# Optimization experiments

Hardware: AMD Instinct MI355X
Metric: run time of the kernel (lower is better)

## Reference

```python
import jax, jax.numpy as jnp
import numpy as np

B, C, H, W = 16, 256, 64, 64
C8, C2 = C // 8, C // 2


def conv1x1(x, w, b):
    # x: [B,Cin,H,W], w: [Cout,Cin], b: [Cout]
    return jnp.einsum('oc,bchw->bohw', w, x) + b[None, :, None, None]


def maxpool2(x):
    # 2x2 max pool, stride 2. x: [B,C,H,W] -> [B,C,H//2,W//2]
    b, c, h, w = x.shape
    return x.reshape(b, c, h // 2, 2, w // 2, 2).max(axis=(3, 5))


def setup_inputs() -> dict:
    key = jax.random.key(0)
    ks = jax.random.split(key, 9)
    s = lambda fan_in: 1.0 / np.sqrt(fan_in)
    return {
        'x': jax.random.normal(ks[0], (B, C, H, W), jnp.float32),
        'w_theta': jax.random.normal(ks[1], (C8, C), jnp.float32) * s(C),
        'b_theta': jax.random.normal(ks[2], (C8,), jnp.float32) * 0.01,
        'w_phi': jax.random.normal(ks[3], (C8, C), jnp.float32) * s(C),
        'b_phi': jax.random.normal(ks[4], (C8,), jnp.float32) * 0.01,
        'w_g': jax.random.normal(ks[5], (C2, C), jnp.float32) * s(C),
        'b_g': jax.random.normal(ks[6], (C2,), jnp.float32) * 0.01,
        'w_o': jax.random.normal(ks[7], (C, C2), jnp.float32) * s(C2),
        'b_o': jax.random.normal(ks[8], (C,), jnp.float32) * 0.01,
        'gamma': jnp.full((1,), 0.5, jnp.float32),
    }


def reference(x, w_theta, b_theta, w_phi, b_phi, w_g, b_g, w_o, b_o, gamma):
    b, c, h, w = x.shape
    n, m = h * w, (h * w) // 4
    theta = conv1x1(x, w_theta, b_theta).reshape(b, C8, n)        # [B,C/8,N]
    phi = maxpool2(conv1x1(x, w_phi, b_phi)).reshape(b, C8, m)    # [B,C/8,M]
    g = maxpool2(conv1x1(x, w_g, b_g)).reshape(b, C2, m)          # [B,C/2,M]
    # beta = softmax(theta^T phi) over keys M
    scores = jnp.einsum('bcn,bcm->bnm', theta, phi)               # [B,N,M]
    beta = jax.nn.softmax(scores, axis=-1)
    o_pre = jnp.einsum('bcm,bnm->bcn', g, beta).reshape(b, C2, h, w)
    o = conv1x1(o_pre, w_o, b_o)                                  # [B,C,H,W]
    return gamma[0] * o + x
```

## Files before the change

kernel.cpp:

```cpp
#include <hip/hip_runtime.h>
#include <hip/hip_bf16.h>

#define BB 16

typedef __attribute__((ext_vector_type(8))) short bf16x8;
typedef __attribute__((ext_vector_type(4))) float f32x4;

__device__ __forceinline__ unsigned short f2bfbits(float f) {
    union { float f; unsigned u; } v; v.f = f;
    unsigned r = v.u + 0x7fffu + ((v.u >> 16) & 1u);
    return (unsigned short)(r >> 16);
}
__device__ __forceinline__ float bfraw(unsigned short u) {
    union { unsigned u; float f; } v; v.u = ((unsigned)u) << 16; return v.f;
}
__device__ __forceinline__ unsigned packbf2(float lo, float hi) {
    return (unsigned)f2bfbits(lo) | ((unsigned)f2bfbits(hi) << 16);
}

__global__ void prep_kernel(
    const float* __restrict__ wt, const float* __restrict__ bt,
    const float* __restrict__ wp, const float* __restrict__ bp,
    const float* __restrict__ wg, const float* __restrict__ bg,
    const float* __restrict__ wo,
    unsigned short* __restrict__ w_all, unsigned short* __restrict__ w_o_bf,
    float* __restrict__ b_all)
{
    int i = blockIdx.x * 256 + threadIdx.x;
    if (i < 8192)        w_all[i] = f2bfbits(wt[i]);
    else if (i < 16384)  w_all[i] = f2bfbits(wp[i - 8192]);
    else if (i < 49152)  w_all[i] = f2bfbits(wg[i - 16384]);
    else if (i < 81920)  w_o_bf[i - 49152] = f2bfbits(wo[i - 49152]);
    else if (i < 82112) {
        int r = i - 81920;
        b_all[r] = (r < 32) ? bt[r] : (r < 64) ? bp[r - 32] : bg[r - 64];
    }
}

__global__ __launch_bounds__(256) void xt_kernel(
    const float* __restrict__ x, unsigned short* __restrict__ x_t)
{
    __shared__ unsigned short lt[64 * 74];

    const int t = threadIdx.x;
    const int bid = blockIdx.x;
    const int b  = bid >> 8;
    const int p0 = ((bid >> 2) & 63) << 6;
    const int c0 = (bid & 3) << 6;

    {
        int c = t & 63, seg = t >> 6;
        const float* src = x + ((size_t)(b * 256 + c0 + c)) * 4096 + p0 + seg * 16;
        #pragma unroll
        for (int j = 0; j < 4; ++j) {
            float4 v = *(const float4*)(src + 4 * j);
            unsigned* dst = (unsigned*)(lt + c * 74 + seg * 16 + 4 * j);
            dst[0] = packbf2(v.x, v.y);
            dst[1] = packbf2(v.z, v.w);
        }
    }
    __syncthreads();
    {
        int p = t >> 2, quad = t & 3;
        #pragma unroll
        for (int h = 0; h < 2; ++h) {
            union { unsigned short u[8]; int4 v; } o;
            #pragma unroll
            for (int e = 0; e < 8; ++e)
                o.u[e] = lt[(quad * 16 + h * 8 + e) * 74 + p];
            *(int4*)(x_t + ((size_t)(b * 4096 + p0 + p)) * 256 + c0 + quad * 16 + h * 8) = o.v;
        }
    }
}

__global__ __launch_bounds__(256, 2) void proj_kernel(
    const unsigned short* __restrict__ x_t,
    const unsigned short* __restrict__ w_all,
    const float* __restrict__ b_all,
    unsigned short* __restrict__ theta_t,
    unsigned short* __restrict__ phi_t,
    unsigned short* __restrict__ g)
{
    __shared__ unsigned short ot[192 * 136];

    const int t = threadIdx.x;
    const int w = t >> 6;
    const int l = t & 63;
    const int lr = l & 15, lg = l >> 4;
    const int b  = blockIdx.x >> 5;
    const int pt = blockIdx.x & 31;
    const int pbase = pt << 7;
    const int mb = pt << 5;

    f32x4 acc[3][8];
    #pragma unroll
    for (int i = 0; i < 3; ++i)
        #pragma unroll
        for (int nt = 0; nt < 8; ++nt) acc[i][nt] = (f32x4){0.f,0.f,0.f,0.f};

    #pragma unroll 1
    for (int ks = 0; ks < 8; ++ks) {
        bf16x8 af[3];
        #pragma unroll
        for (int i = 0; i < 3; ++i)
            af[i] = *(const bf16x8*)(w_all + (size_t)(16*(3*w+i) + lr)*256 + 32*ks + 8*lg);
        #pragma unroll
        for (int nt = 0; nt < 8; ++nt) {
            bf16x8 bx = *(const bf16x8*)(x_t + ((size_t)(b*4096 + pbase + 16*nt + lr))*256 + 32*ks + 8*lg);
            #pragma unroll
            for (int i = 0; i < 3; ++i)
                acc[i][nt] = __builtin_amdgcn_mfma_f32_16x16x32_bf16(af[i], bx, acc[i][nt], 0, 0, 0);
        }
    }

    float bias[3][4];
    #pragma unroll
    for (int i = 0; i < 3; ++i)
        #pragma unroll
        for (int r = 0; r < 4; ++r) bias[i][r] = b_all[16*(3*w+i) + 4*lg + r];
    #pragma unroll
    for (int i = 0; i < 3; ++i)
        #pragma unroll
        for (int nt = 0; nt < 8; ++nt)
            #pragma unroll
            for (int r = 0; r < 4; ++r)
                ot[(16*(3*w+i) + 4*lg + r)*136 + 16*nt + lr] =
                    f2bfbits(acc[i][nt][r] + bias[i][r]);
    __syncthreads();

    if (t < 128) {
        int p = t;
        union { unsigned short u[32]; int4 v[4]; } th;
        #pragma unroll
        for (int c = 0; c < 32; ++c) th.u[c] = ot[c*136 + p];
        int4* dst = (int4*)(theta_t + ((size_t)(b*4096 + pbase + p)) * 32);
        #pragma unroll
        for (int q = 0; q < 4; ++q) dst[q] = th.v[q];
    }
    {
        int ww = t >> 3, c0 = (t & 7) * 4;
        union { unsigned short u[4]; int2 v; } ph;
        #pragma unroll
        for (int e = 0; e < 4; ++e) {
            int row = 32 + c0 + e;
            unsigned p01 = *(const unsigned*)&ot[row*136 + 2*ww];
            unsigned p23 = *(const unsigned*)&ot[row*136 + 64 + 2*ww];
            float m0 = fmaxf(bfraw((unsigned short)p01), bfraw((unsigned short)(p01 >> 16)));
            float m1 = fmaxf(bfraw((unsigned short)p23), bfraw((unsigned short)(p23 >> 16)));
            ph.u[e] = f2bfbits(fmaxf(m0, m1));
        }
        *(int2*)(phi_t + ((size_t)(b*1024 + mb + ww)) * 32 + c0) = ph.v;
    }
    {
        int c2 = t >> 1, w0 = (t & 1) * 16;
        int row = 64 + c2;
        union { unsigned short u[16]; int4 v[2]; } gv;
        #pragma unroll
        for (int e = 0; e < 16; ++e) {
            int ww = w0 + e;
            unsigned p01 = *(const unsigned*)&ot[row*136 + 2*ww];
            unsigned p23 = *(const unsigned*)&ot[row*136 + 64 + 2*ww];
            float m0 = fmaxf(bfraw((unsigned short)p01), bfraw((unsigned short)(p01 >> 16)));
            float m1 = fmaxf(bfraw((unsigned short)p23), bfraw((unsigned short)(p23 >> 16)));
            gv.u[e] = f2bfbits(fmaxf(m0, m1));
        }
        int4* dst = (int4*)(g + ((size_t)(b*128 + c2)) * 1024 + mb + w0);
        dst[0] = gv.v[0]; dst[1] = gv.v[1];
    }
}

__global__ __launch_bounds__(256, 4) void attn_kernel(
    const unsigned short* __restrict__ theta_t,
    const unsigned short* __restrict__ phi_t,
    const unsigned short* __restrict__ g,
    unsigned short* __restrict__ o_pre_t)
{
    __shared__ unsigned short plds[4][16 * 72];
    __shared__ unsigned short olds[4][16 * 136];

    const int t = threadIdx.x;
    const int wv = t >> 6;
    const int l  = t & 63;
    const int lr = l & 15, lg = l >> 4;
    const int b   = blockIdx.x >> 6;
    const int nq0 = (blockIdx.x & 63) * 64 + wv * 16;

    const f32x4 zero = {0.f, 0.f, 0.f, 0.f};

    const bf16x8 aq = *(const bf16x8*)(theta_t + ((size_t)(b*4096 + nq0 + lr))*32 + 8*lg);

    f32x4 po[8];
    #pragma unroll
    for (int ct = 0; ct < 8; ++ct) po[ct] = zero;
    float m_run = -1e30f, l_run = 0.f;

    const unsigned short* phb = phi_t + (size_t)b * 1024 * 32;
    const unsigned short* gb  = g + (size_t)b * 128 * 1024;
    unsigned short* pw = plds[wv];

    #pragma unroll 1
    for (int kt = 0; kt < 16; ++kt) {
        const int mb = kt * 64;
        f32x4 s[4];
        #pragma unroll
        for (int mt = 0; mt < 4; ++mt) {
            bf16x8 ap = *(const bf16x8*)(phb + (size_t)(mb + 16*mt + lr)*32 + 8*lg);
            s[mt] = __builtin_amdgcn_mfma_f32_16x16x32_bf16(ap, aq, zero, 0, 0, 0);
        }
        float mx = -1e30f;
        #pragma unroll
        for (int mt = 0; mt < 4; ++mt)
            #pragma unroll
            for (int r = 0; r < 4; ++r) mx = fmaxf(mx, s[mt][r]);
        mx = fmaxf(mx, __shfl_xor(mx, 16));
        mx = fmaxf(mx, __shfl_xor(mx, 32));
        float nm = fmaxf(m_run, mx);
        float sc = __expf(m_run - nm);
        float ls = 0.f;
        #pragma unroll
        for (int mt = 0; mt < 4; ++mt)
            #pragma unroll
            for (int r = 0; r < 4; ++r) {
                float p = __expf(s[mt][r] - nm);
                s[mt][r] = p; ls += p;
            }
        ls += __shfl_xor(ls, 16);
        ls += __shfl_xor(ls, 32);
        l_run = l_run * sc + ls;
        m_run = nm;
        float scB[4];
        #pragma unroll
        for (int r = 0; r < 4; ++r) scB[r] = __shfl(sc, 4*lg + r);
        #pragma unroll
        for (int ct = 0; ct < 8; ++ct)
            #pragma unroll
            for (int r = 0; r < 4; ++r) po[ct][r] *= scB[r];
        #pragma unroll
        for (int mt = 0; mt < 4; ++mt)
            #pragma unroll
            for (int i = 0; i < 2; ++i)
                *(unsigned*)(pw + lr*72 + 16*mt + 4*lg + 2*i) =
                    packbf2(s[mt][2*i], s[mt][2*i + 1]);
        #pragma unroll
        for (int ks = 0; ks < 2; ++ks) {
            bf16x8 pa = *(const bf16x8*)(pw + lr*72 + 32*ks + 8*lg);
            #pragma unroll
            for (int ct = 0; ct < 8; ++ct) {
                bf16x8 bgv = *(const bf16x8*)(gb + (size_t)(16*ct + lr)*1024 + mb + 32*ks + 8*lg);
                po[ct] = __builtin_amdgcn_mfma_f32_16x16x32_bf16(pa, bgv, po[ct], 0, 0, 0);
            }
        }
    }

    float invq = 1.f / l_run;
    float invB[4];
    #pragma unroll
    for (int r = 0; r < 4; ++r) invB[r] = __shfl(invq, 4*lg + r);
    unsigned short* ow = olds[wv];
    #pragma unroll
    for (int ct = 0; ct < 8; ++ct)
        #pragma unroll
        for (int r = 0; r < 4; ++r)
            ow[(4*lg + r)*136 + 16*ct + lr] = f2bfbits(po[ct][r] * invB[r]);
    #pragma unroll
    for (int i = 0; i < 4; ++i) {
        int q = 4*i + lg;
        int4 v = *(const int4*)(ow + q*136 + 8*lr);
        *(int4*)(o_pre_t + ((size_t)(b*4096 + nq0 + q))*128 + 8*lr) = v;
    }
}

__global__ __launch_bounds__(256, 2) void out_kernel(
    const unsigned short* __restrict__ o_pre_t,
    const unsigned short* __restrict__ w_o_bf,
    const float* __restrict__ b_o,
    const float* __restrict__ x,
    const float* __restrict__ gamma,
    float* __restrict__ out)
{
    const int t = threadIdx.x;
    const int w = t >> 6, l = t & 63;
    const int lr = l & 15, lg = l >> 4;
    const int b   = blockIdx.x >> 6;
    const int nbv = (blockIdx.x & 63) << 6;

    f32x4 acc[4][4];
    #pragma unroll
    for (int i = 0; i < 4; ++i)
        #pragma unroll
        for (int nt = 0; nt < 4; ++nt) acc[i][nt] = (f32x4){0.f,0.f,0.f,0.f};

    #pragma unroll 1
    for (int ks = 0; ks < 4; ++ks) {
        bf16x8 aw[4], bo[4];
        #pragma unroll
        for (int i = 0; i < 4; ++i)
            aw[i] = *(const bf16x8*)(w_o_bf + (size_t)(16*(4*w+i) + lr)*128 + 32*ks + 8*lg);
        #pragma unroll
        for (int nt = 0; nt < 4; ++nt)
            bo[nt] = *(const bf16x8*)(o_pre_t + ((size_t)(b*4096 + nbv + 16*nt + lr))*128 + 32*ks + 8*lg);
        #pragma unroll
        for (int i = 0; i < 4; ++i)
            #pragma unroll
            for (int nt = 0; nt < 4; ++nt)
                acc[i][nt] = __builtin_amdgcn_mfma_f32_16x16x32_bf16(aw[i], bo[nt], acc[i][nt], 0, 0, 0);
    }

    const float gam = gamma[0];
    float bias[4][4];
    #pragma unroll
    for (int i = 0; i < 4; ++i)
        #pragma unroll
        for (int r = 0; r < 4; ++r) bias[i][r] = b_o[16*(4*w+i) + 4*lg + r];

    #pragma unroll
    for (int i = 0; i < 4; ++i)
        #pragma unroll
        for (int nt = 0; nt < 4; ++nt)
            #pragma unroll
            for (int r = 0; r < 4; ++r) {
                int co = 16*(4*w+i) + 4*lg + r;
                int n  = nbv + 16*nt + lr;
                size_t off = ((size_t)(b*256 + co)) * 4096 + n;
                out[off] = gam * (acc[i][nt][r] + bias[i][r]) + x[off];
            }
}

extern "C" void kernel_launch(void* const* d_in, const int* in_sizes, int n_in,
                              void* d_out, int out_size, void* d_ws, size_t ws_size,
                              hipStream_t stream)
{
    const float* x       = (const float*)d_in[0];
    const float* w_theta = (const float*)d_in[1];
    const float* b_theta = (const float*)d_in[2];
    const float* w_phi   = (const float*)d_in[3];
    const float* b_phi   = (const float*)d_in[4];
    const float* w_g     = (const float*)d_in[5];
    const float* b_g     = (const float*)d_in[6];
    const float* w_o     = (const float*)d_in[7];
    const float* b_o     = (const float*)d_in[8];
    const float* gamma   = (const float*)d_in[9];
    float* outp = (float*)d_out;

    char* ws = (char*)d_ws;
    unsigned short* w_all   = (unsigned short*)ws;
    unsigned short* w_o_bf  = (unsigned short*)(ws + 98304);
    float*          b_all   = (float*)(ws + 163840);
    unsigned short* x_t     = (unsigned short*)(ws + (1u << 20));
    unsigned short* o_pre_t = (unsigned short*)(ws + (1u << 20));
    unsigned short* theta_t = (unsigned short*)(ws + (33u << 20));
    unsigned short* phi_t   = (unsigned short*)(ws + (37u << 20));
    unsigned short* g       = (unsigned short*)(ws + (38u << 20));

    prep_kernel<<<321, 256, 0, stream>>>(w_theta, b_theta, w_phi, b_phi,
                                         w_g, b_g, w_o, w_all, w_o_bf, b_all);
    xt_kernel<<<BB * 256, 256, 0, stream>>>(x, x_t);
    proj_kernel<<<BB * 32, 256, 0, stream>>>(x_t, w_all, b_all, theta_t, phi_t, g);
    attn_kernel<<<BB * 64, 256, 0, stream>>>(theta_t, phi_t, g, o_pre_t);
    out_kernel<<<BB * 64, 256, 0, stream>>>(o_pre_t, w_o_bf, b_o, x, gamma, outp);
}
```

Baseline: 315.1 us.

## Process two query tiles per wave in attention and prefetch phi/g operands

The attention kernel now gives each wave 32 queries (two 16-row tiles) instead of 16, so every g and phi fragment loaded from global memory is reused across two query tiles, and the grid is halved. The g fragments for each key tile are loaded into registers at the top of the iteration, and phi for the next tile is prefetched, so load latency can overlap with compute. Launch bounds drop to 2 blocks per CU to fit the larger register footprint. The proj and out kernels also get their k-loop unrolled by 2. The cost is higher register pressure, lower occupancy, and only 512 attention blocks.

```diff
diff --git a/kernel.cpp b/kernel.cpp
--- a/kernel.cpp
+++ b/kernel.cpp
@@ -98,7 +98,7 @@
         #pragma unroll
         for (int nt = 0; nt < 8; ++nt) acc[i][nt] = (f32x4){0.f,0.f,0.f,0.f};
 
-    #pragma unroll 1
+    #pragma unroll 2
     for (int ks = 0; ks < 8; ++ks) {
         bf16x8 af[3];
         #pragma unroll
@@ -169,101 +169,141 @@
     }
 }
 
-__global__ __launch_bounds__(256, 4) void attn_kernel(
+__global__ __launch_bounds__(256, 2) void attn_kernel(
     const unsigned short* __restrict__ theta_t,
     const unsigned short* __restrict__ phi_t,
     const unsigned short* __restrict__ g,
     unsigned short* __restrict__ o_pre_t)
 {
-    __shared__ unsigned short plds[4][16 * 72];
-    __shared__ unsigned short olds[4][16 * 136];
+    __shared__ unsigned short plds[4][32 * 72];
+    __shared__ unsigned short olds[4][32 * 136];
 
     const int t = threadIdx.x;
     const int wv = t >> 6;
     const int l  = t & 63;
     const int lr = l & 15, lg = l >> 4;
-    const int b   = blockIdx.x >> 6;
-    const int nq0 = (blockIdx.x & 63) * 64 + wv * 16;
+    const int b   = blockIdx.x >> 5;
+    const int nq0 = (blockIdx.x & 31) * 128 + wv * 32;
 
     const f32x4 zero = {0.f, 0.f, 0.f, 0.f};
 
-    const bf16x8 aq = *(const bf16x8*)(theta_t + ((size_t)(b*4096 + nq0 + lr))*32 + 8*lg);
-
-    f32x4 po[8];
-    #pragma unroll
-    for (int ct = 0; ct < 8; ++ct) po[ct] = zero;
-    float m_run = -1e30f, l_run = 0.f;
+    bf16x8 aq[2];
+    #pragma unroll
+    for (int qt = 0; qt < 2; ++qt)
+        aq[qt] = *(const bf16x8*)(theta_t + ((size_t)(b*4096 + nq0 + 16*qt + lr))*32 + 8*lg);
+
+    f32x4 po[2][8];
+    #pragma unroll
+    for (int qt = 0; qt < 2; ++qt)
+        #pragma unroll
+        for (int ct = 0; ct < 8; ++ct) po[qt][ct] = zero;
+    float m_run[2] = {-1e30f, -1e30f}, l_run[2] = {0.f, 0.f};
 
     const unsigned short* phb = phi_t + (size_t)b * 1024 * 32;
     const unsigned short* gb  = g + (size_t)b * 128 * 1024;
     unsigned short* pw = plds[wv];
 
+    bf16x8 pf[4];
+    #pragma unroll
+    for (int mt = 0; mt < 4; ++mt)
+        pf[mt] = *(const bf16x8*)(phb + (size_t)(16*mt + lr)*32 + 8*lg);
+
     #pragma unroll 1
     for (int kt = 0; kt < 16; ++kt) {
         const int mb = kt * 64;
-        f32x4 s[4];
+        bf16x8 gv[16];
+        #pragma unroll
+        for (int ks = 0; ks < 2; ++ks)
+            #pragma unroll
+            for (int ct = 0; ct < 8; ++ct)
+                gv[ks*8 + ct] = *(const bf16x8*)(gb + (size_t)(16*ct + lr)*1024 + mb + 32*ks + 8*lg);
+
+        f32x4 s[2][4];
         #pragma unroll
         for (int mt = 0; mt < 4; ++mt) {
-            bf16x8 ap = *(const bf16x8*)(phb + (size_t)(mb + 16*mt + lr)*32 + 8*lg);
-            s[mt] = __builtin_amdgcn_mfma_f32_16x16x32_bf16(ap, aq, zero, 0, 0, 0);
-        }
-        float mx = -1e30f;
-        #pragma unroll
-        for (int mt = 0; mt < 4; ++mt)
-            #pragma unroll
-            for (int r = 0; r < 4; ++r) mx = fmaxf(mx, s[mt][r]);
-        mx = fmaxf(mx, __shfl_xor(mx, 16));
-        mx = fmaxf(mx, __shfl_xor(mx, 32));
-        float nm = fmaxf(m_run, mx);
-        float sc = __expf(m_run - nm);
-        float ls = 0.f;
-        #pragma unroll
-        for (int mt = 0; mt < 4; ++mt)
-            #pragma unroll
-            for (int r = 0; r < 4; ++r) {
-                float p = __expf(s[mt][r] - nm);
-                s[mt][r] = p; ls += p;
+            s[0][mt] = __builtin_amdgcn_mfma_f32_16x16x32_bf16(pf[mt], aq[0], zero, 0, 0, 0);
+            s[1][mt] = __builtin_amdgcn_mfma_f32_16x16x32_bf16(pf[mt], aq[1], zero, 0, 0, 0);
+        }
+        {
+            const int mbn = (kt < 15) ? mb + 64 : mb;
+            #pragma unroll
+            for (int mt = 0; mt < 4; ++mt)
+                pf[mt] = *(const bf16x8*)(phb + (size_t)(mbn + 16*mt + lr)*32 + 8*lg);
+        }
+
+        float scv[2];
+        #pragma unroll
+        for (int qt = 0; qt < 2; ++qt) {
+            float mx = -1e30f;
+            #pragma unroll
+            for (int mt = 0; mt < 4; ++mt)
+                #pragma unroll
+                for (int r = 0; r < 4; ++r) mx = fmaxf(mx, s[qt][mt][r]);
+            mx = fmaxf(mx, __shfl_xor(mx, 16));
+            mx = fmaxf(mx, __shfl_xor(mx, 32));
+            float nm = fmaxf(m_run[qt], mx);
+            float sc = __expf(m_run[qt] - nm);
+            float ls = 0.f;
+            #pragma unroll
+            for (int mt = 0; mt < 4; ++mt)
+                #pragma unroll
+                for (int r = 0; r < 4; ++r) {
+                    float p = __expf(s[qt][mt][r] - nm);
+                    s[qt][mt][r] = p; ls += p;
+                }
+            ls += __shfl_xor(ls, 16);
+            ls += __shfl_xor(ls, 32);
+            l_run[qt] = l_run[qt] * sc + ls;
+            m_run[qt] = nm;
+            scv[qt] = sc;
+        }
+        #pragma unroll
+        for (int qt = 0; qt < 2; ++qt) {
+            float scB[4];
+            #pragma unroll
+            for (int r = 0; r < 4; ++r) scB[r] = __shfl(scv[qt], 4*lg + r);
+            #pragma unroll
+            for (int ct = 0; ct < 8; ++ct)
+                #pragma unroll
+                for (int r = 0; r < 4; ++r) po[qt][ct][r] *= scB[r];
+        }
+        #pragma unroll
+        for (int qt = 0; qt < 2; ++qt)
+            #pragma unroll
+            for (int mt = 0; mt < 4; ++mt)
+                #pragma unroll
+                for (int i = 0; i < 2; ++i)
+                    *(unsigned*)(pw + (16*qt + lr)*72 + 16*mt + 4*lg + 2*i) =
+                        packbf2(s[qt][mt][2*i], s[qt][mt][2*i + 1]);
+        #pragma unroll
+        for (int ks = 0; ks < 2; ++ks) {
+            bf16x8 pa0 = *(const bf16x8*)(pw + (size_t)lr*72 + 32*ks + 8*lg);
+            bf16x8 pa1 = *(const bf16x8*)(pw + (size_t)(16 + lr)*72 + 32*ks + 8*lg);
+            #pragma unroll
+            for (int ct = 0; ct < 8; ++ct) {
+                po[0][ct] = __builtin_amdgcn_mfma_f32_16x16x32_bf16(pa0, gv[ks*8+ct], po[0][ct], 0, 0, 0);
+                po[1][ct] = __builtin_amdgcn_mfma_f32_16x16x32_bf16(pa1, gv[ks*8+ct], po[1][ct], 0, 0, 0);
             }
-        ls += __shfl_xor(ls, 16);
-        ls += __shfl_xor(ls, 32);
-        l_run = l_run * sc + ls;
-        m_run = nm;
-        float scB[4];
-        #pragma unroll
-        for (int r = 0; r < 4; ++r) scB[r] = __shfl(sc, 4*lg + r);
+        }
+    }
+
+    float invB[2][4];
+    #pragma unroll
+    for (int qt = 0; qt < 2; ++qt) {
+        float invq = 1.f / l_run[qt];
+        #pragma unroll
+        for (int r = 0; r < 4; ++r) invB[qt][r] = __shfl(invq, 4*lg + r);
+    }
+    unsigned short* ow = olds[wv];
+    #pragma unroll
+    for (int qt = 0; qt < 2; ++qt)
         #pragma unroll
         for (int ct = 0; ct < 8; ++ct)
             #pragma unroll
-            for (int r = 0; r < 4; ++r) po[ct][r] *= scB[r];
-        #pragma unroll
-        for (int mt = 0; mt < 4; ++mt)
-            #pragma unroll
-            for (int i = 0; i < 2; ++i)
-                *(unsigned*)(pw + lr*72 + 16*mt + 4*lg + 2*i) =
-                    packbf2(s[mt][2*i], s[mt][2*i + 1]);
-        #pragma unroll
-        for (int ks = 0; ks < 2; ++ks) {
-            bf16x8 pa = *(const bf16x8*)(pw + lr*72 + 32*ks + 8*lg);
-            #pragma unroll
-            for (int ct = 0; ct < 8; ++ct) {
-                bf16x8 bgv = *(const bf16x8*)(gb + (size_t)(16*ct + lr)*1024 + mb + 32*ks + 8*lg);
-                po[ct] = __builtin_amdgcn_mfma_f32_16x16x32_bf16(pa, bgv, po[ct], 0, 0, 0);
-            }
-        }
-    }
-
-    float invq = 1.f / l_run;
-    float invB[4];
-    #pragma unroll
-    for (int r = 0; r < 4; ++r) invB[r] = __shfl(invq, 4*lg + r);
-    unsigned short* ow = olds[wv];
-    #pragma unroll
-    for (int ct = 0; ct < 8; ++ct)
-        #pragma unroll
-        for (int r = 0; r < 4; ++r)
-            ow[(4*lg + r)*136 + 16*ct + lr] = f2bfbits(po[ct][r] * invB[r]);
-    #pragma unroll
-    for (int i = 0; i < 4; ++i) {
+            for (int r = 0; r < 4; ++r)
+                ow[(16*qt + 4*lg + r)*136 + 16*ct + lr] = f2bfbits(po[qt][ct][r] * invB[qt][r]);
+    #pragma unroll
+    for (int i = 0; i < 8; ++i) {
         int q = 4*i + lg;
         int4 v = *(const int4*)(ow + q*136 + 8*lr);
         *(int4*)(o_pre_t + ((size_t)(b*4096 + nq0 + q))*128 + 8*lr) = v;
@@ -290,7 +330,7 @@
         #pragma unroll
         for (int nt = 0; nt < 4; ++nt) acc[i][nt] = (f32x4){0.f,0.f,0.f,0.f};
 
-    #pragma unroll 1
+    #pragma unroll 2
     for (int ks = 0; ks < 4; ++ks) {
         bf16x8 aw[4], bo[4];
         #pragma unroll
@@ -356,6 +396,6 @@
                                          w_g, b_g, w_o, w_all, w_o_bf, b_all);
     xt_kernel<<<BB * 256, 256, 0, stream>>>(x, x_t);
     proj_kernel<<<BB * 32, 256, 0, stream>>>(x_t, w_all, b_all, theta_t, phi_t, g);
-    attn_kernel<<<BB * 64, 256, 0, stream>>>(theta_t, phi_t, g, o_pre_t);
+    attn_kernel<<<BB * 32, 256, 0, stream>>>(theta_t, phi_t, g, o_pre_t);
     out_kernel<<<BB * 64, 256, 0, stream>>>(o_pre_t, w_o_bf, b_o, x, gamma, outp);
 }
```

Measured after the change: 262.1 us. -16.8%, faster.
